# Performance work log

Hardware: AMD Instinct MI355X
Metric: run time of the kernel (lower is better)

Reference implementation:

```python
import jax, jax.numpy as jnp
import numpy as np

B, N, C, H, KH = 4, 4096, 1024, 16, 5
HD = C // H  # head dim = 64


def setup_inputs() -> dict:
    key = jax.random.key(0)
    ks = jax.random.split(key, 4)
    return {
        "x": jax.random.normal(ks[0], (B, N, C), jnp.float32),
        "qkv_w": jax.random.normal(ks[1], (3 * C, C), jnp.float32) * 0.02,
        "qkv_b": jnp.zeros((3 * C,), jnp.float32),
        "proj_w": jax.random.normal(ks[2], (C, C), jnp.float32) * 0.02,
        "proj_b": jnp.zeros((C,), jnp.float32),
        "pos_enc": jnp.zeros((1, C), jnp.float32),  # torch init: zeros
        "dwc_w": jax.random.normal(ks[3], (HD, 1, KH, KH), jnp.float32) * 0.05,
        "dwc_b": jnp.zeros((HD,), jnp.float32),
        "num_heads": H,
    }


def reference(x, qkv_w, qkv_b, proj_w, proj_b, pos_enc, dwc_w, dwc_b, num_heads):
    b, n, c = x.shape
    h = num_heads
    hd = c // h
    kh = dwc_w.shape[2]

    qkv = x @ qkv_w.T + qkv_b                     # (b, n, 3c)
    q, k, v = jnp.split(qkv, 3, axis=-1)          # each (b, n, c)
    k = k + pos_enc[:, :c]                        # broadcast (1, c)
    q = jax.nn.relu(q)
    k = jax.nn.relu(k)

    def to_heads(t):  # (b, n, c) -> (b*h, n, hd)
        return t.reshape(b, n, h, hd).transpose(0, 2, 1, 3).reshape(b * h, n, hd)

    q, k, v = to_heads(q), to_heads(k), to_heads(v)

    # linear attention in fp32 (inputs already fp32)
    z = 1.0 / (jnp.einsum('bic,bc->bi', q, k.sum(axis=1)) + 1e-6)   # (bh, n)
    kv = jnp.einsum('bjc,bjd->bcd', k, v)                           # (bh, hd, hd)
    out = jnp.einsum('bic,bcd->bid', q, kv) * z[:, :, None]         # (bh, n, hd)

    # depthwise 2D conv on v viewed as (bh, hd, n, 1), kernel (hd,1,kh,kh), pad kh//2
    fm = v.transpose(0, 2, 1)[..., None]                            # (bh, hd, n, 1)
    pad = kh // 2
    fm = jax.lax.conv_general_dilated(
        fm, dwc_w, window_strides=(1, 1),
        padding=((pad, pad), (pad, pad)),
        dimension_numbers=('NCHW', 'OIHW', 'NCHW'),
        feature_group_count=hd,
    ) + dwc_b[None, :, None, None]
    out = out + fm[..., 0].transpose(0, 2, 1)                       # (bh, n, hd)

    out = out.reshape(b, h, n, hd).transpose(0, 2, 1, 3).reshape(b, n, c)
    return out @ proj_w.T + proj_b
```

## Files before the change

kernel.cpp:

```cpp
#include <hip/hip_runtime.h>


#define BB   4
#define NN   4096
#define CDIM 1024
#define NH   16
#define HDIM 64
#define BH   64

typedef __attribute__((ext_vector_type(8))) short short8;
typedef __attribute__((ext_vector_type(4))) float f32x4;
typedef unsigned short u16;

__device__ __forceinline__ float b2f(short s) {
    union { unsigned u; float f; } c;
    c.u = ((unsigned)(unsigned short)s) << 16;
    return c.f;
}
__device__ __forceinline__ u16 f2b(float f) {
    unsigned u = __float_as_uint(f);
    return (u16)((u + 0x7fffu + ((u >> 16) & 1u)) >> 16);
}
__device__ __forceinline__ void gload16(const void* g, void* l) {
    __builtin_amdgcn_global_load_lds((const __attribute__((address_space(1))) void*)g,
                                     (__attribute__((address_space(3))) void*)l, 16, 0, 0);
}

__global__ __launch_bounds__(256) void k_fill_diag(float* __restrict__ out, int n, float val)
{
    int i = blockIdx.x * 256 + threadIdx.x;
    if (i < n) out[i] = val;
}

__global__ __launch_bounds__(256) void k_convert_all(
    const float* __restrict__ x, const float* __restrict__ qw, const float* __restrict__ pw,
    u16* __restrict__ xb, u16* __restrict__ qwb, u16* __restrict__ pwb)
{
    int i = blockIdx.x * 256 + threadIdx.x;
    const float* src; u16* dst; int j;
    if (i < 4194304)      { src = x;  dst = xb;  j = i; }
    else if (i < 4980736) { src = qw; dst = qwb; j = i - 4194304; }
    else                  { src = pw; dst = pwb; j = i - 4980736; }
    float4 v = reinterpret_cast<const float4*>(src)[j];
    ushort4 o;
    o.x = f2b(v.x); o.y = f2b(v.y); o.z = f2b(v.z); o.w = f2b(v.w);
    reinterpret_cast<ushort4*>(dst)[j] = o;
}

#define GEMM256_2BAR()                                                                   \
    const int t = threadIdx.x;                                                           \
    const int l = t & 63, w = t >> 6;                                                    \
    const int wr = w >> 2, wc = w & 3;                                                   \
    const int fr = l & 15;                                                               \
    const int physE  = ((l >> 4) ^ ((fr >> 1) & 3)) * 8;                                 \
    const int qa     = ((l & 3) ^ ((l >> 3) & 3)) * 8;                                   \
    const int aRow   = w * 16 + (l >> 2);                                                \
    const u16* gA0 = A  + (size_t)(brow + aRow) * 1024 + qa;                             \
    const u16* gB0 = Bw + (size_t)(bcol + aRow) * 1024 + qa;                             \
    char* ldsc = (char*)lds;                                                             \
    const int afBase = (wr * 128 + fr) * 32 + physE;                                     \
    const int bfBase = 16384 + (wc * 64 + fr) * 32 + physE;                              \
    f32x4 acc[8][4];                                                                     \
    _Pragma("unroll")                                                                    \
    for (int m = 0; m < 8; ++m)                                                          \
        _Pragma("unroll")                                                                \
        for (int n = 0; n < 4; ++n) acc[m][n] = (f32x4){0.f, 0.f, 0.f, 0.f};             \
    auto STG = [&](int kt, int kh, int isB) {                                            \
        const u16* g = (isB ? gB0 : gA0) + kt * 64 + kh * 32;                            \
        char* d = ldsc + (kt & 1) * 65536 + isB * 32768 + kh * 16384 + w * 1024 + l * 16;\
        gload16(g,          d);                                                          \
        gload16(g + 131072, d + 8192);                                                   \
    };                                                                                   \
    STG(0,0,0); STG(0,0,1); STG(0,1,0); STG(0,1,1); STG(1,0,0); STG(1,0,1);              \
    asm volatile("s_waitcnt vmcnt(4)" ::: "memory");                                     \
    __builtin_amdgcn_s_barrier();                                                        \
    _Pragma("unroll 1")                                                                  \
    for (int kt = 0; kt < 16; ++kt) {                                                    \
        const int B0 = (kt & 1) * 32768;                                                 \
        short8 af[8], bf[4];                                                             \
                                                             \
        _Pragma("unroll")                                                                \
        for (int n = 0; n < 4; ++n)                                                      \
            bf[n] = *reinterpret_cast<const short8*>(&lds[B0 + bfBase + n * 512]);       \
        _Pragma("unroll")                                                                \
        for (int m = 0; m < 8; ++m)                                                      \
            af[m] = *reinterpret_cast<const short8*>(&lds[B0 + afBase + m * 512]);       \
        if (kt + 1 < 16) { STG(kt + 1, 1, 0); STG(kt + 1, 1, 1); }                       \
        __builtin_amdgcn_s_setprio(1);                                                   \
        _Pragma("unroll")                                                                \
        for (int m = 0; m < 8; ++m)                                                      \
            _Pragma("unroll")                                                            \
            for (int n = 0; n < 4; ++n)                                                  \
                acc[m][n] = __builtin_amdgcn_mfma_f32_16x16x32_bf16(af[m], bf[n], acc[m][n], 0, 0, 0); \
        __builtin_amdgcn_s_setprio(0);                                                   \
        __builtin_amdgcn_s_barrier();        \
                                                             \
        _Pragma("unroll")                                                                \
        for (int n = 0; n < 4; ++n)                                                      \
            bf[n] = *reinterpret_cast<const short8*>(&lds[B0 + 8192 + bfBase + n * 512]);\
        _Pragma("unroll")                                                                \
        for (int m = 0; m < 8; ++m)                                                      \
            af[m] = *reinterpret_cast<const short8*>(&lds[B0 + 8192 + afBase + m * 512]);\
        if (kt + 2 < 16) { STG(kt + 2, 0, 0); STG(kt + 2, 0, 1); }                       \
        __builtin_amdgcn_s_setprio(1);                                                   \
        _Pragma("unroll")                                                                \
        for (int m = 0; m < 8; ++m)                                                      \
            _Pragma("unroll")                                                            \
            for (int n = 0; n < 4; ++n)                                                  \
                acc[m][n] = __builtin_amdgcn_mfma_f32_16x16x32_bf16(af[m], bf[n], acc[m][n], 0, 0, 0); \
        __builtin_amdgcn_s_setprio(0);                                                   \
        if (kt < 15) { asm volatile("s_waitcnt vmcnt(4)" ::: "memory"); }                \
        else         { asm volatile("s_waitcnt vmcnt(0)" ::: "memory"); }                \
        __builtin_amdgcn_s_barrier();                \
    }

__global__ __launch_bounds__(512, 2) void k_gemm1_256(
    const u16* __restrict__ A, const u16* __restrict__ Bw,
    const float* __restrict__ bias, const float* __restrict__ pos_enc,
    u16* __restrict__ q, u16* __restrict__ ktg, u16* __restrict__ v, u16* __restrict__ vtg)
{
    __shared__ u16 lds[65536];
    const int lid = blockIdx.y * 12 + blockIdx.x;
    const int swz = (lid & 7) * 96 + (lid >> 3);
    const int bcol = (swz % 12) * 256;
    const int brow = (swz / 12) * 256;

    GEMM256_2BAR()

    const int part = bcol >> 10;
    {
        const int row_l = wr * 128 + (l >> 4) * 4;
        const int col_l = wc * 64 + fr;
        #pragma unroll
        for (int n = 0; n < 4; ++n) {
            const int col = col_l + n * 16;
            const int gc = bcol + col;
            const int c = gc & 1023;
            float bv = bias[gc];
            if (part == 1) bv += pos_enc[c];
            const int cc = col >> 3, in = col & 7;
            #pragma unroll
            for (int m = 0; m < 8; ++m)
                #pragma unroll
                for (int j = 0; j < 4; ++j) {
                    const int row = row_l + m * 16 + j;
                    float val = acc[m][n][j] + bv;
                    if (part != 2) val = fmaxf(val, 0.f);
                    lds[row * 256 + ((cc ^ (row & 7)) << 3) + in] = f2b(val);
                }
        }
    }
    __syncthreads();
    const int b_ = brow >> 12, i0 = brow & 4095;
    if (part != 1) {
        u16* dst = (part == 0) ? q : v;
        #pragma unroll
        for (int it = 0; it < 16; ++it) {
            const int id = it * 512 + t;
            const int row = id >> 5, cc = id & 31;
            short8 val = *reinterpret_cast<const short8*>(&lds[row * 256 + ((cc ^ (row & 7)) << 3)]);
            const int c2 = (bcol + cc * 8) & 1023;
            const int h2 = c2 >> 6, d2 = c2 & 63;
            *reinterpret_cast<short8*>(
                &dst[((size_t)(b_ * NH + h2) * NN + i0 + row) * HDIM + d2]) = val;
        }
    }
    if (part != 0) {
        u16* dstT = (part == 1) ? ktg : vtg;
        #pragma unroll
        for (int it = 0; it < 16; ++it) {
            const int id = it * 512 + t;
            const int cl = id & 255, jc = id >> 8;
            short8 vv;
            #pragma unroll
            for (int rr = 0; rr < 8; ++rr)
                vv[rr] = (short)lds[(jc * 8 + rr) * 256 + (((cl >> 3) ^ rr) << 3) + (cl & 7)];
            const int c2 = (bcol + cl) & 1023;
            const int h2 = c2 >> 6, d2 = c2 & 63;
            *reinterpret_cast<short8*>(
                &dstT[((size_t)(b_ * NH + h2) * HDIM + d2) * NN + i0 + jc * 8]) = vv;
        }
    }
}

__global__ __launch_bounds__(512, 2) void k_gemm2_256(
    const u16* __restrict__ A, const u16* __restrict__ Bw,
    const float* __restrict__ bias, float* __restrict__ out)
{
    __shared__ u16 lds[65536];
    const int lid = blockIdx.y * 4 + blockIdx.x;
    const int swz = (lid & 7) * 32 + (lid >> 3);
    const int bcol = (swz % 4) * 256;
    const int brow = (swz / 4) * 256;

    GEMM256_2BAR()

    float* ldsf = reinterpret_cast<float*>(lds);
    #pragma unroll 1
    for (int half = 0; half < 2; ++half) {
        __syncthreads();
        if (wr == half) {
            const int row_l = (l >> 4) * 4;
            const int col_l = wc * 64 + fr;
            #pragma unroll
            for (int n = 0; n < 4; ++n) {
                const int col = col_l + n * 16;
                const float bv = bias[bcol + col];
                #pragma unroll
                for (int m = 0; m < 8; ++m)
                    #pragma unroll
                    for (int j = 0; j < 4; ++j) {
                        const int row = m * 16 + row_l + j;
                        ldsf[row * 256 + (col ^ (((row >> 2) & 3) << 3))] = acc[m][n][j] + bv;
                    }
            }
        }
        __syncthreads();
        const float4* ldsf4 = reinterpret_cast<const float4*>(ldsf);
        #pragma unroll
        for (int it = 0; it < 16; ++it) {
            const int id = it * 512 + t;
            const int row = id >> 6, cc4 = id & 63;
            float4 vv = ldsf4[row * 64 + (cc4 ^ (((row >> 2) & 3) << 1))];
            *reinterpret_cast<float4*>(
                &out[(size_t)(brow + half * 128 + row) * CDIM + bcol + cc4 * 4]) = vv;
        }
    }
}

__global__ __launch_bounds__(256) void k_kv_mfma(
    const u16* __restrict__ ktg, const u16* __restrict__ vtg,
    float* __restrict__ part)
{
    __shared__ float red[4][5120];
    const int t = threadIdx.x, l = t & 63, w = t >> 6;
    const int bh = blockIdx.x, ch = blockIdx.y;
    const u16* kb = ktg + (size_t)bh * HDIM * NN;
    const u16* vb = vtg + (size_t)bh * HDIM * NN;
    const int j0 = ch * 1024 + w * 256;
    const int fr = l & 15, kf = (l >> 4) * 8;

    f32x4 acc[5][4];
    #pragma unroll
    for (int m = 0; m < 5; ++m)
        #pragma unroll
        for (int n = 0; n < 4; ++n) acc[m][n] = (f32x4){0.f, 0.f, 0.f, 0.f};
    short8 ones;
    #pragma unroll
    for (int i = 0; i < 8; ++i) ones[i] = (short)0x3F80;

    for (int js = 0; js < 256; js += 32) {
        const int jb = j0 + js + kf;
        short8 a[4], b[4];
        #pragma unroll
        for (int m = 0; m < 4; ++m)
            a[m] = *reinterpret_cast<const short8*>(&vb[(size_t)(m * 16 + fr) * NN + jb]);
        #pragma unroll
        for (int n = 0; n < 4; ++n)
            b[n] = *reinterpret_cast<const short8*>(&kb[(size_t)(n * 16 + fr) * NN + jb]);
        #pragma unroll
        for (int m = 0; m < 4; ++m)
            #pragma unroll
            for (int n = 0; n < 4; ++n)
                acc[m][n] = __builtin_amdgcn_mfma_f32_16x16x32_bf16(a[m], b[n], acc[m][n], 0, 0, 0);
        #pragma unroll
        for (int n = 0; n < 4; ++n)
            acc[4][n] = __builtin_amdgcn_mfma_f32_16x16x32_bf16(ones, b[n], acc[4][n], 0, 0, 0);
    }
    #pragma unroll
    for (int m = 0; m < 5; ++m)
        #pragma unroll
        for (int n = 0; n < 4; ++n)
            #pragma unroll
            for (int j = 0; j < 4; ++j)
                red[w][(m * 16 + (l >> 4) * 4 + j) * 64 + fr + n * 16] = acc[m][n][j];
    __syncthreads();
    float* po = part + ((size_t)ch * BH + bh) * 5120;
    for (int i = t; i < 5120; i += 256)
        po[i] = red[0][i] + red[1][i] + red[2][i] + red[3][i];
}

__global__ __launch_bounds__(256) void k_kv_red(
    const float* __restrict__ part, u16* __restrict__ kvt)
{
    const int bh = blockIdx.x, t = threadIdx.x;
    u16* base = kvt + bh * 5120;
    for (int i = t; i < 5120; i += 256) {
        float s = part[(size_t)(0 * BH + bh) * 5120 + i]
                + part[(size_t)(1 * BH + bh) * 5120 + i]
                + part[(size_t)(2 * BH + bh) * 5120 + i]
                + part[(size_t)(3 * BH + bh) * 5120 + i];
        base[i] = f2b(s);
    }
}

__global__ __launch_bounds__(256) void k_attn_mfma(
    const u16* __restrict__ q, const u16* __restrict__ v,
    const u16* __restrict__ kvt,
    const float* __restrict__ dwc_w, const float* __restrict__ dwc_b,
    u16* __restrict__ out2)
{
    __shared__ u16 att[4][64 * 68];
    const int t = threadIdx.x;
    const int l = t & 63, w = t >> 6;
    const int bh = blockIdx.x;
    const int tb = blockIdx.y * 256 + w * 64;
    const size_t hb = (size_t)bh * NN * HDIM;
    const u16* qb  = q + hb + (size_t)tb * HDIM;
    const u16* kvb = kvt + bh * 5120;

    const int fr = l & 15;
    const int kfrag = (l >> 4) * 8;

    short8 bfr[5][2];
    #pragma unroll
    for (int n = 0; n < 5; ++n)
        #pragma unroll
        for (int ks = 0; ks < 2; ++ks)
            bfr[n][ks] = *reinterpret_cast<const short8*>(&kvb[(n * 16 + fr) * 64 + ks * 32 + kfrag]);

    f32x4 acc[4][5];
    #pragma unroll
    for (int m = 0; m < 4; ++m)
        #pragma unroll
        for (int n = 0; n < 5; ++n) acc[m][n] = (f32x4){0.f, 0.f, 0.f, 0.f};

    #pragma unroll
    for (int m = 0; m < 4; ++m)
        #pragma unroll
        for (int ks = 0; ks < 2; ++ks) {
            short8 a = *reinterpret_cast<const short8*>(&qb[(m * 16 + fr) * 64 + ks * 32 + kfrag]);
            #pragma unroll
            for (int n = 0; n < 5; ++n)
                acc[m][n] = __builtin_amdgcn_mfma_f32_16x16x32_bf16(a, bfr[n][ks], acc[m][n], 0, 0, 0);
        }

    #pragma unroll
    for (int m = 0; m < 4; ++m)
        #pragma unroll
        for (int j = 0; j < 4; ++j) {
            const float den = __shfl(acc[m][4][j], l & 48);
            const float z = 1.f / (den + 1e-6f);
            const int row = m * 16 + (l >> 4) * 4 + j;
            #pragma unroll
            for (int n = 0; n < 4; ++n)
                att[w][row * 68 + fr + n * 16] = f2b(acc[m][n][j] * z);
        }
    __syncthreads();

    const int d = l;
    float w5[5];
    #pragma unroll
    for (int dh = 0; dh < 5; ++dh) w5[dh] = dwc_w[d * 25 + dh * 5 + 2];
    const float cbias = dwc_b[d];
    const int b_ = bh >> 4, h_ = bh & 15;
    u16* obase = out2 + (size_t)b_ * NN * CDIM + (size_t)h_ * 64 + d;
    float win[5];
    #pragma unroll
    for (int p = 0; p < 4; ++p) {
        const int src = tb - 2 + p;
        win[p] = (src >= 0 && src < NN) ? b2f(v[hb + (size_t)src * 64 + d]) : 0.f;
    }
    for (int it = 0; it < 64; ++it) {
        const int srcn = tb + it + 2;
        win[4] = (srcn < NN) ? b2f(v[hb + (size_t)srcn * 64 + d]) : 0.f;
        const float fm = cbias + w5[0] * win[0] + w5[1] * win[1] + w5[2] * win[2]
                               + w5[3] * win[3] + w5[4] * win[4];
        const float attn = b2f((short)att[w][it * 68 + d]);
        obase[(size_t)(tb + it) * CDIM] = f2b(attn + fm);
        win[0] = win[1]; win[1] = win[2]; win[2] = win[3]; win[3] = win[4];
    }
}

extern "C" void kernel_launch(void* const* d_in, const int* in_sizes, int n_in,
                              void* d_out, int out_size, void* d_ws, size_t ws_size,
                              hipStream_t stream)
{
    const float* x       = (const float*)d_in[0];
    const float* qkv_w   = (const float*)d_in[1];
    const float* qkv_b   = (const float*)d_in[2];
    const float* proj_w  = (const float*)d_in[3];
    const float* proj_b  = (const float*)d_in[4];
    const float* pos_enc = (const float*)d_in[5];
    const float* dwc_w   = (const float*)d_in[6];
    const float* dwc_b   = (const float*)d_in[7];

    const size_t QKV = 16777216;
    char* p = (char*)d_ws;
    u16* q_b    = (u16*)p;               p += QKV * 2;
    u16* ktg    = (u16*)p;               p += QKV * 2;
    u16* v_b    = (u16*)p;               p += QKV * 2;
    u16* vtg    = (u16*)p;               p += QKV * 2;
    u16* x_b    = (u16*)p;               p += QKV * 2;
    u16* qkvw_b = (u16*)p;               p += (size_t)3145728 * 2;
    u16* projw_b= (u16*)p;               p += (size_t)1048576 * 2;
    float* part = (float*)p;             p += (size_t)4 * BH * 5120 * 4;
    u16* kvt    = (u16*)p;               p += (size_t)(BH * 5120) * 2;
    const size_t need_bytes = (size_t)(p - (char*)d_ws);

    if (ws_size < need_bytes) {
        const float diag = 4096.0f + (float)(ws_size >> 20);
        k_fill_diag<<<(out_size + 255) / 256, 256, 0, stream>>>((float*)d_out, out_size, diag);
        return;
    }

    u16* out2 = ktg;
    float* out = (float*)d_out;

    k_convert_all<<<20480, 256, 0, stream>>>(x, qkv_w, proj_w, x_b, qkvw_b, projw_b);

    k_gemm1_256 <<<dim3(12, 64), 512, 0, stream>>>(x_b, qkvw_b, qkv_b, pos_enc, q_b, ktg, v_b, vtg);
    k_kv_mfma   <<<dim3(64, 4),  256, 0, stream>>>(ktg, vtg, part);
    k_kv_red    <<<64,           256, 0, stream>>>(part, kvt);
    k_attn_mfma <<<dim3(64, 16), 256, 0, stream>>>(q_b, v_b, kvt, dwc_w, dwc_b, out2);
    k_gemm2_256 <<<dim3(4, 64),  512, 0, stream>>>(out2, projw_b, proj_b, out);
}
```

Before: 276.0 us.

## Double-buffer MFMA fragments in registers and deepen global prefetch in GEMMs

Both bf16 GEMM kernels now read the next half-tile's LDS fragments into a second register set before issuing the MFMAs for the current half. This overlaps LDS reads with matrix math instead of stalling on them. The prologue now stages the whole second k-tile, so wait counts move to vmcnt(8) and global loads run deeper ahead. The cost is about double the fragment registers under launch_bounds(512,2), which risks spills or lower occupancy.

```diff
diff --git a/kernel.cpp b/kernel.cpp
--- a/kernel.cpp
+++ b/kernel.cpp
@@ -47,7 +47,24 @@
     reinterpret_cast<ushort4*>(dst)[j] = o;
 }
 
-#define GEMM256_2BAR()                                                                   \
+#define RD_FRAGS(AF, BF, OFF)                                                            \
+    _Pragma("unroll")                                                                    \
+    for (int n = 0; n < 4; ++n)                                                          \
+        BF[n] = *reinterpret_cast<const short8*>(&lds[(OFF) + bfBase + n * 512]);        \
+    _Pragma("unroll")                                                                    \
+    for (int m = 0; m < 8; ++m)                                                          \
+        AF[m] = *reinterpret_cast<const short8*>(&lds[(OFF) + afBase + m * 512]);
+
+#define DO_MFMA(AF, BF)                                                                  \
+    __builtin_amdgcn_s_setprio(1);                                                       \
+    _Pragma("unroll")                                                                    \
+    for (int m = 0; m < 8; ++m)                                                          \
+        _Pragma("unroll")                                                                \
+        for (int n = 0; n < 4; ++n)                                                      \
+            acc[m][n] = __builtin_amdgcn_mfma_f32_16x16x32_bf16(AF[m], BF[n], acc[m][n], 0, 0, 0); \
+    __builtin_amdgcn_s_setprio(0);
+
+#define GEMM256_RPIPE()                                                                  \
     const int t = threadIdx.x;                                                           \
     const int l = t & 63, w = t >> 6;                                                    \
     const int wr = w >> 2, wc = w & 3;                                                   \
@@ -71,47 +88,29 @@
         gload16(g,          d);                                                          \
         gload16(g + 131072, d + 8192);                                                   \
     };                                                                                   \
-    STG(0,0,0); STG(0,0,1); STG(0,1,0); STG(0,1,1); STG(1,0,0); STG(1,0,1);              \
-    asm volatile("s_waitcnt vmcnt(4)" ::: "memory");                                     \
+    STG(0,0,0); STG(0,0,1); STG(0,1,0); STG(0,1,1);                                      \
+    STG(1,0,0); STG(1,0,1); STG(1,1,0); STG(1,1,1);                                      \
+    asm volatile("s_waitcnt vmcnt(8)" ::: "memory");                                     \
     __builtin_amdgcn_s_barrier();                                                        \
+    short8 afA[8], bfA[4], afB[8], bfB[4];                                               \
+    RD_FRAGS(afA, bfA, 0)                                             \
     _Pragma("unroll 1")                                                                  \
     for (int kt = 0; kt < 16; ++kt) {                                                    \
         const int B0 = (kt & 1) * 32768;                                                 \
-        short8 af[8], bf[4];                                                             \
-                                                             \
-        _Pragma("unroll")                                                                \
-        for (int n = 0; n < 4; ++n)                                                      \
-            bf[n] = *reinterpret_cast<const short8*>(&lds[B0 + bfBase + n * 512]);       \
-        _Pragma("unroll")                                                                \
-        for (int m = 0; m < 8; ++m)                                                      \
-            af[m] = *reinterpret_cast<const short8*>(&lds[B0 + afBase + m * 512]);       \
-        if (kt + 1 < 16) { STG(kt + 1, 1, 0); STG(kt + 1, 1, 1); }                       \
-        __builtin_amdgcn_s_setprio(1);                                                   \
-        _Pragma("unroll")                                                                \
-        for (int m = 0; m < 8; ++m)                                                      \
-            _Pragma("unroll")                                                            \
-            for (int n = 0; n < 4; ++n)                                                  \
-                acc[m][n] = __builtin_amdgcn_mfma_f32_16x16x32_bf16(af[m], bf[n], acc[m][n], 0, 0, 0); \
-        __builtin_amdgcn_s_setprio(0);                                                   \
-        __builtin_amdgcn_s_barrier();        \
-                                                             \
-        _Pragma("unroll")                                                                \
-        for (int n = 0; n < 4; ++n)                                                      \
-            bf[n] = *reinterpret_cast<const short8*>(&lds[B0 + 8192 + bfBase + n * 512]);\
-        _Pragma("unroll")                                                                \
-        for (int m = 0; m < 8; ++m)                                                      \
-            af[m] = *reinterpret_cast<const short8*>(&lds[B0 + 8192 + afBase + m * 512]);\
+        const int B1 = B0 ^ 32768;                                                       \
+                        \
+        RD_FRAGS(afB, bfB, B0 + 8192)                                                    \
         if (kt + 2 < 16) { STG(kt + 2, 0, 0); STG(kt + 2, 0, 1); }                       \
-        __builtin_amdgcn_s_setprio(1);                                                   \
-        _Pragma("unroll")                                                                \
-        for (int m = 0; m < 8; ++m)                                                      \
-            _Pragma("unroll")                                                            \
-            for (int n = 0; n < 4; ++n)                                                  \
-                acc[m][n] = __builtin_amdgcn_mfma_f32_16x16x32_bf16(af[m], bf[n], acc[m][n], 0, 0, 0); \
-        __builtin_amdgcn_s_setprio(0);                                                   \
-        if (kt < 15) { asm volatile("s_waitcnt vmcnt(4)" ::: "memory"); }                \
+        DO_MFMA(afA, bfA)                                                                \
+        asm volatile("s_waitcnt vmcnt(8)" ::: "memory");                                 \
+        __builtin_amdgcn_s_barrier();                                           \
+                      \
+        if (kt + 1 < 16) { RD_FRAGS(afA, bfA, B1) }                                      \
+        if (kt + 2 < 16) { STG(kt + 2, 1, 0); STG(kt + 2, 1, 1); }                       \
+        DO_MFMA(afB, bfB)                                                                \
+        if (kt < 15) { asm volatile("s_waitcnt vmcnt(8)" ::: "memory"); }                \
         else         { asm volatile("s_waitcnt vmcnt(0)" ::: "memory"); }                \
-        __builtin_amdgcn_s_barrier();                \
+        __builtin_amdgcn_s_barrier();                                           \
     }
 
 __global__ __launch_bounds__(512, 2) void k_gemm1_256(
@@ -125,7 +124,7 @@
     const int bcol = (swz % 12) * 256;
     const int brow = (swz / 12) * 256;
 
-    GEMM256_2BAR()
+    GEMM256_RPIPE()
 
     const int part = bcol >> 10;
     {
@@ -193,7 +192,7 @@
     const int bcol = (swz % 4) * 256;
     const int brow = (swz / 4) * 256;
 
-    GEMM256_2BAR()
+    GEMM256_RPIPE()
 
     float* ldsf = reinterpret_cast<float*>(lds);
     #pragma unroll 1
```

Result: slower. 282.6 us (+2.4%).
